# Performance work log

Hardware: AMD Instinct MI355X
Metric: run time of the kernel (lower is better)

## Reference

```python
import jax, jax.numpy as jnp
import numpy as np

CH = 50        # channel
RED = 2        # reduction -> match channels = 25
KS = 3         # ksize
SM_SCALE = 10.0
SCALES = [1.0, 0.9, 0.8, 0.7, 0.6]
ESCAPE_NAN = 1e-4


def prelu(x, a):
    return jnp.where(x >= 0, x, a * x)


def conv1x1(x, w, b):
    # x: [B,Ci,H,W], w: [Co,Ci], b: [Co]
    return jnp.einsum('bihw,oi->bohw', x, w) + b[None, :, None, None]


def patches3(x):
    # extract 3x3 stride-1 SAME patches, torch-unfold (C,kh,kw) ordering
    # x: [B,C,H,W] -> [B, H*W, C, 3, 3]
    B, C, H, W = x.shape
    p = jnp.pad(x, ((0, 0), (0, 0), (1, 1), (1, 1)))
    cols = jnp.stack([p[:, :, i:i + H, j:j + W]
                      for i in range(KS) for j in range(KS)], axis=2)  # [B,C,9,H,W]
    cols = cols.reshape(B, C, KS, KS, H * W)
    return cols.transpose(0, 4, 1, 2, 3)


def setup_inputs() -> dict:
    key = jax.random.key(0)
    ks = jax.random.split(key, 7)
    B, H, W = 4, 48, 48
    f = CH // RED  # 25
    s1 = 1.0 / np.sqrt(CH)
    return {
        'x': jax.random.normal(ks[0], (B, CH, H, W), jnp.float32),
        # conv_match_L_base: 1x1 conv CH->f + PReLU
        'w_base': jax.random.normal(ks[1], (f, CH), jnp.float32) * s1,
        'b_base': jnp.zeros((f,), jnp.float32),
        'a_base': jnp.float32(0.25),
        # conv_match: 1x1 conv CH->f + PReLU
        'w_match': jax.random.normal(ks[2], (f, CH), jnp.float32) * s1,
        'b_match': jnp.zeros((f,), jnp.float32),
        'a_match': jnp.float32(0.25),
        # conv_assembly: 1x1 conv CH->CH + PReLU
        'w_asm': jax.random.normal(ks[3], (CH, CH), jnp.float32) * s1,
        'b_asm': jnp.zeros((CH,), jnp.float32),
        'a_asm': jnp.float32(0.25),
    }


def reference(x, w_base, b_base, a_base, w_match, b_match, a_match,
              w_asm, b_asm, a_asm):
    B, C, H, W = x.shape
    match_base = prelu(conv1x1(x, w_base, b_base), a_base)  # [B,25,H,W]

    w_list, raw_list = [], []
    for s in SCALES:
        if s == 1.0:
            ref = x
        else:
            Hs, Ws = int(H * s), int(W * s)
            ref = jax.image.resize(x, (B, C, Hs, Ws), method='cubic')
        base = prelu(conv1x1(ref, w_asm, b_asm), a_asm)       # [B,C,Hs,Ws]
        raw_list.append(patches3(base))                       # [B,Hs*Ws,C,3,3]
        refm = prelu(conv1x1(ref, w_match, b_match), a_match)  # [B,25,Hs,Ws]
        w_list.append(patches3(refm))                         # [B,Hs*Ws,25,3,3]

    wi = jnp.concatenate(w_list, axis=1)    # [B, L, 25, 3, 3]
    raw = jnp.concatenate(raw_list, axis=1)  # [B, L, C, 3, 3]

    def attend(xb, wb, rb):
        # xb: [25,H,W]; wb: [L,25,3,3]; rb: [L,C,3,3]
        norm = jnp.maximum(
            jnp.sqrt(jnp.sum(wb * wb, axis=(1, 2, 3), keepdims=True)),
            ESCAPE_NAN)
        wn = wb / norm
        score = jax.lax.conv_general_dilated(
            xb[None], wn, (1, 1), [(1, 1), (1, 1)])[0]        # [L,H,W]
        attn = jax.nn.softmax(score * SM_SCALE, axis=0)
        # conv_transpose2d(stride=1, pad=1) == corr with flipped, transposed kernel
        wt = jnp.flip(rb, axis=(2, 3)).transpose(1, 0, 2, 3)  # [C,L,3,3]
        out = jax.lax.conv_general_dilated(
            attn[None], wt, (1, 1), [(1, 1), (1, 1)])[0]      # [C,H,W]
        return out * 0.25

    y = jax.vmap(attend)(match_base, wi, raw)
    return y + x  # res_scale = 1
```

## Files before the change

### kernel.cpp

```cpp
#include <hip/hip_runtime.h>
#include <hip/hip_bf16.h>
#include <math.h>


#define L_TOT 7470
#define L_PAD 7680
#define NCHUNK 4
#define CHUNK_TILES 30
#define KD    256
#define JD    512
#define HW    2304

typedef unsigned short u16;
typedef __attribute__((ext_vector_type(8))) short bf16x8;
typedef __attribute__((ext_vector_type(4))) float f32x4;

__device__ inline u16 f2b(float f) {
    __hip_bfloat16 h = __float2bfloat16(f);
    return __builtin_bit_cast(u16, h);
}
__device__ inline float b2f(u16 u) {
    __hip_bfloat16 h = __builtin_bit_cast(__hip_bfloat16, u);
    return __bfloat162float(h);
}

__constant__ int c_hs[5]   = {48, 43, 38, 33, 28};
__constant__ int c_loff[6] = {0, 2304, 4153, 5597, 6686, 7470};

#define GLOAD16(g, l) __builtin_amdgcn_global_load_lds(                          \
        (__attribute__((address_space(1))) const void*)(g),                      \
        (__attribute__((address_space(3))) void*)(l), 16, 0, 0)

__global__ void prep_kernel(float* __restrict__ wmall, int* __restrict__ dtab) {
    int r = blockIdx.x * 256 + threadIdx.x;
    if (r < 142) {
        int sizes[4] = {43, 38, 33, 28};
        int si = 0, i = r, woffs = 0;
        for (si = 0; si < 4; ++si) {
            if (i < sizes[si]) break;
            i -= sizes[si];
            woffs += sizes[si] * 48;
        }
        int osz = sizes[si];
        float inv_scale = 48.0f / (float)osz;
        float kscale = inv_scale;
        float sample_f = ((float)i + 0.5f) * inv_scale - 0.5f;
        float w[48];
        float tot = 0.f;
        for (int j = 0; j < 48; ++j) {
            float t = fabsf(sample_f - (float)j) / kscale;
            float v;
            if (t >= 2.f)       v = 0.f;
            else if (t >= 1.f)  v = ((-0.5f * t + 2.5f) * t - 4.f) * t + 2.f;
            else                v = ((1.5f * t - 2.5f) * t) * t + 1.f;
            w[j] = v;
            tot += v;
        }
        float invt = 1.f / tot;
        for (int j = 0; j < 48; ++j) wmall[woffs + i * 48 + j] = w[j] * invt;
    }
    if (r < L_PAD) {
        int v;
        if (r >= L_TOT) v = (int)0x80000000u;
        else {
            int si = 0;
#pragma unroll
            for (int s = 0; s < 4; ++s)
                if (r >= c_loff[s + 1]) si = s + 1;
            int pos = r - c_loff[si];
            int hs = c_hs[si];
            int ly = pos / hs, lx = pos % hs;
            v = si | (ly << 4) | (lx << 10);
        }
        dtab[r] = v;
    }
}

__global__ void resize_h_all(const float* __restrict__ in, const float* __restrict__ wm,
                             float* __restrict__ t1, float* __restrict__ t2,
                             float* __restrict__ t3, float* __restrict__ t4) {
    int idx = blockIdx.x * 256 + threadIdx.x;
    int rem = idx, osz, woffm;
    float* tmp;
    if (rem < 200 * 43 * 48) { osz = 43; tmp = t1; woffm = 0; }
    else {
        rem -= 200 * 43 * 48;
        if (rem < 200 * 38 * 48) { osz = 38; tmp = t2; woffm = 43 * 48; }
        else {
            rem -= 200 * 38 * 48;
            if (rem < 200 * 33 * 48) { osz = 33; tmp = t3; woffm = (43 + 38) * 48; }
            else {
                rem -= 200 * 33 * 48;
                if (rem >= 200 * 28 * 48) return;
                osz = 28; tmp = t4; woffm = (43 + 38 + 33) * 48;
            }
        }
    }
    int xi = rem % 48;
    int t = rem / 48;
    int yo = t % osz;
    int bc = t / osz;
    const float* wr = wm + (size_t)(woffm + yo * 48);
    const float* ip = in + (size_t)bc * 2304 + xi;
    float s = 0.f;
#pragma unroll
    for (int yi = 0; yi < 48; ++yi) s += wr[yi] * ip[yi * 48];
    tmp[rem] = s;
}

__global__ void resize_w_all(const float* __restrict__ t1, const float* __restrict__ t2,
                             const float* __restrict__ t3, const float* __restrict__ t4,
                             const float* __restrict__ wm,
                             float* __restrict__ r1, float* __restrict__ r2,
                             float* __restrict__ r3, float* __restrict__ r4) {
    int idx = blockIdx.x * 256 + threadIdx.x;
    int rem = idx, osz, woffm;
    const float* tmp;
    float* outp;
    if (rem < 200 * 43 * 43) { osz = 43; tmp = t1; outp = r1; woffm = 0; }
    else {
        rem -= 200 * 43 * 43;
        if (rem < 200 * 38 * 38) { osz = 38; tmp = t2; outp = r2; woffm = 43 * 48; }
        else {
            rem -= 200 * 38 * 38;
            if (rem < 200 * 33 * 33) { osz = 33; tmp = t3; outp = r3; woffm = (43 + 38) * 48; }
            else {
                rem -= 200 * 33 * 33;
                if (rem >= 200 * 28 * 28) return;
                osz = 28; tmp = t4; outp = r4; woffm = (43 + 38 + 33) * 48;
            }
        }
    }
    int xo = rem % osz;
    int t = rem / osz;
    int yo = t % osz;
    int bc = t / osz;
    const float* wr = wm + (size_t)(woffm + xo * 48);
    const float* ip = tmp + ((size_t)bc * osz + yo) * 48;
    float s = 0.f;
#pragma unroll
    for (int xi = 0; xi < 48; ++xi) s += wr[xi] * ip[xi];
    outp[rem] = s;
}

__global__ void conv_all(const float* __restrict__ x,
                         const float* __restrict__ r1, const float* __restrict__ r2,
                         const float* __restrict__ r3, const float* __restrict__ r4,
                         const float* __restrict__ w_asm, const float* __restrict__ b_asm,
                         const float* __restrict__ a_asm,
                         const float* __restrict__ w_match, const float* __restrict__ b_match,
                         const float* __restrict__ a_match,
                         const float* __restrict__ w_base, const float* __restrict__ b_base,
                         const float* __restrict__ a_base,
                         float* __restrict__ base_out, float* __restrict__ refm_out,
                         float* __restrict__ mb_out) {
    int idx = blockIdx.x * 256 + threadIdx.x;
    int rem = idx, P, loffv, NCO;
    const float* in;
    if (rem < 400 * 2304) { P = 2304; in = x; loffv = 0; NCO = 100; }
    else {
        rem -= 400 * 2304;
        if (rem < 300 * 1849) { P = 1849; in = r1; loffv = 2304; NCO = 75; }
        else {
            rem -= 300 * 1849;
            if (rem < 300 * 1444) { P = 1444; in = r2; loffv = 4153; NCO = 75; }
            else {
                rem -= 300 * 1444;
                if (rem < 300 * 1089) { P = 1089; in = r3; loffv = 5597; NCO = 75; }
                else {
                    rem -= 300 * 1089;
                    if (rem >= 300 * 784) return;
                    P = 784; in = r4; loffv = 6686; NCO = 75;
                }
            }
        }
    }
    int p = rem % P;
    int t = rem / P;
    int co = t % NCO;
    int b = t / NCO;
    const float* ip = in + (size_t)b * 50 * P + p;
    const float* wr;
    float bias, av;
    float* outp;
    if (co < 50) {
        wr = w_asm + co * 50; bias = b_asm[co]; av = a_asm[0];
        outp = base_out + (size_t)200 * loffv + ((size_t)(b * 50 + co)) * P + p;
    } else if (co < 75) {
        int cm = co - 50;
        wr = w_match + cm * 50; bias = b_match[cm]; av = a_match[0];
        outp = refm_out + (size_t)100 * loffv + ((size_t)(b * 25 + cm)) * P + p;
    } else {
        int cm = co - 75;
        wr = w_base + cm * 50; bias = b_base[cm]; av = a_base[0];
        outp = mb_out + ((size_t)(b * 25 + cm)) * P + p;
    }
    float s = bias;
#pragma unroll
    for (int ci = 0; ci < 50; ++ci) s += wr[ci] * ip[(size_t)ci * P];
    *outp = (s >= 0.f) ? s : av * s;
}

__global__ void q_build(const float* __restrict__ mb, u16* __restrict__ Q) {
    int idx = blockIdx.x * 256 + threadIdx.x;
    if (idx >= 4 * HW * 25) return;
    int c = idx % 25;
    int t = idx / 25;
    int p = t % HW;
    int b = t / HW;
    int y = p / 48, xx = p % 48;
    const float* rc = mb + (size_t)(b * 25 + c) * HW;
    u16 ov[9];
#pragma unroll
    for (int ky = 0; ky < 3; ++ky)
#pragma unroll
        for (int kx = 0; kx < 3; ++kx) {
            int yy = y + ky - 1, xv = xx + kx - 1;
            float v = (yy >= 0 && yy < 48 && xv >= 0 && xv < 48) ? rc[yy * 48 + xv] : 0.f;
            ov[ky * 3 + kx] = f2b(v);
        }
    u16* dst = Q + (size_t)(b * HW + p) * KD + c * 9;
#pragma unroll
    for (int r = 0; r < 9; ++r) dst[r] = ov[r];
    if (c == 24) {
        u16* z = dst + 9;
#pragma unroll
        for (int i = 0; i < 31; ++i) z[i] = 0;
    }
}

__global__ void norms_kernel(const float* __restrict__ refm_all, const int* __restrict__ dtab,
                             float* __restrict__ norms) {
    int idx = blockIdx.x * 256 + threadIdx.x;
    if (idx >= 4 * L_PAD) return;
    int l = idx % L_PAD;
    int b = idx / L_PAD;
    int d = dtab[l];
    if (d < 0) return;
    int si = d & 15, ly = (d >> 4) & 63, lx = (d >> 10) & 63;
    int hs = c_hs[si], P = hs * hs;
    const float* rb = refm_all + (size_t)100 * c_loff[si] + (size_t)(b * 25) * P;
    float ss = 0.f;
    for (int c = 0; c < 25; ++c) {
        const float* rc = rb + (size_t)c * P;
#pragma unroll
        for (int ky = 0; ky < 3; ++ky)
#pragma unroll
            for (int kx = 0; kx < 3; ++kx) {
                int yy = ly + ky - 1, xv = lx + kx - 1;
                if (yy >= 0 && yy < hs && xv >= 0 && xv < hs) {
                    float v = rc[yy * hs + xv];
                    ss += v * v;
                }
            }
    }
    norms[(size_t)b * L_PAD + l] = 10.0f / fmaxf(sqrtf(ss), 1e-4f);
}

__global__ void kt_build(const float* __restrict__ refm_all, const int* __restrict__ dtab,
                         const float* __restrict__ norms, u16* __restrict__ K) {
    int idx = blockIdx.x * 256 + threadIdx.x;
    if (idx >= 4 * L_PAD * 25) return;
    int c = idx % 25;
    int t = idx / 25;
    int l = t % L_PAD;
    int b = t / L_PAD;
    u16 ov[9] = {0, 0, 0, 0, 0, 0, 0, 0, 0};
    int d = dtab[l];
    if (d >= 0) {
        int si = d & 15, ly = (d >> 4) & 63, lx = (d >> 10) & 63;
        int hs = c_hs[si], P = hs * hs;
        float nrm = norms[(size_t)b * L_PAD + l];
        const float* rc = refm_all + (size_t)100 * c_loff[si] + (size_t)(b * 25 + c) * P;
#pragma unroll
        for (int ky = 0; ky < 3; ++ky)
#pragma unroll
            for (int kx = 0; kx < 3; ++kx) {
                int yy = ly + ky - 1, xv = lx + kx - 1;
                if (yy >= 0 && yy < hs && xv >= 0 && xv < hs)
                    ov[ky * 3 + kx] = f2b(rc[yy * hs + xv] * nrm);
            }
    }
    u16* dst = K + (size_t)(b * L_PAD + l) * KD + c * 9;
#pragma unroll
    for (int r = 0; r < 9; ++r) dst[r] = ov[r];
    if (c == 24) {
        u16* z = dst + 9;
#pragma unroll
        for (int i = 0; i < 31; ++i) z[i] = 0;
    }
}

__global__ void v_build(const float* __restrict__ base_all, const int* __restrict__ dtab,
                        u16* __restrict__ VT) {
    int idx = blockIdx.x * 256 + threadIdx.x;
    if (idx >= 4 * JD * (L_PAD / 8)) return;
    int l8 = idx % (L_PAD / 8);
    int t = idx / (L_PAD / 8);
    int j = t % JD;
    int b = t / JD;
    int l0 = l8 * 8;
    bf16x8 ov = (bf16x8){0, 0, 0, 0, 0, 0, 0, 0};
    if (j < 450) {
        int c = j / 9, r = j % 9, ky = r / 3, kx = r % 3;
#pragma unroll
        for (int u = 0; u < 8; ++u) {
            int d = dtab[l0 + u];
            float v = 0.f;
            if (d >= 0) {
                int si = d & 15, ly = (d >> 4) & 63, lx = (d >> 10) & 63;
                int hs = c_hs[si], P = hs * hs;
                int yy = ly + ky - 1, xv = lx + kx - 1;
                if (yy >= 0 && yy < hs && xv >= 0 && xv < hs)
                    v = base_all[(size_t)200 * c_loff[si] + (size_t)(b * 50 + c) * P + yy * hs + xv];
            }
            ov[u] = (short)f2b(v);
        }
    }
    *(bf16x8*)&VT[(size_t)(b * JD + j) * L_PAD + l0] = ov;
}

__global__ __launch_bounds__(256, 4) void attn_score(
    const u16* __restrict__ Qg, const u16* __restrict__ Kg,
    u16* __restrict__ Ag, float* __restrict__ mC, float* __restrict__ dC) {
    __shared__ u16 smem[64 * KD];
    __shared__ float sm_m[2][64], sm_d[2][64];
    const int bx = blockIdx.x, by = blockIdx.y;
    const int mt = by % 36, zq = by / 36;
    const int z16 = bx + 8 * zq;
    const int b = z16 >> 2, chunk = z16 & 3;
    const int bm = mt * 64;
    const u16* Q = Qg + (size_t)b * HW * KD;
    const u16* K = Kg + (size_t)b * L_PAD * KD;
    u16* A = Ag + (size_t)b * HW * L_PAD;
    const int tid = threadIdx.x, lane = tid & 63, wid = tid >> 6;
    const int wr = wid >> 1, wc = wid & 1;
    const int l15 = lane & 15, l16 = lane >> 4;
    const int l7 = lane & 7;
    const int r_lo = lane >> 5;
    const int u_dst = lane & 31;

    {
        const u16* qrow = Q + (size_t)(bm + wid * 16 + r_lo) * KD;
        u16* qdst = smem + (size_t)(wid * 16) * KD;
#pragma unroll
        for (int q = 0; q < 8; ++q) {
            int sw = (u_dst ^ ((q * 2 + r_lo) & 7)) * 8;
            GLOAD16(qrow + (size_t)(q * 2) * KD + sw, qdst + (q * 2) * KD);
        }
    }
    __syncthreads();
    bf16x8 qf[2][8];
#pragma unroll
    for (int m = 0; m < 2; ++m)
#pragma unroll
        for (int k = 0; k < 8; ++k)
            qf[m][k] = *(const bf16x8*)&smem[(size_t)(wr * 32 + m * 16 + l15) * KD
                                             + (((k * 4 + l16) ^ l7) * 8)];
    __syncthreads();

    float mrun[2][4];
#pragma unroll
    for (int m = 0; m < 2; ++m)
#pragma unroll
        for (int r = 0; r < 4; ++r) mrun[m][r] = -3e38f;

    const int t0 = chunk * CHUNK_TILES;
    const int colb_base = wc * 32 + l15;

    for (int t = t0; t < t0 + CHUNK_TILES; ++t) {
        {
            const u16* krow = K + (size_t)(t * 64 + wid * 16 + r_lo) * KD;
            u16* kdst = smem + (size_t)(wid * 16) * KD;
#pragma unroll
            for (int q = 0; q < 8; ++q) {
                int sw = (u_dst ^ ((q * 2 + r_lo) & 7)) * 8;
                GLOAD16(krow + (size_t)(q * 2) * KD + sw, kdst + (q * 2) * KD);
            }
        }
        __syncthreads();
        f32x4 acc[2][2];
#pragma unroll
        for (int m = 0; m < 2; ++m)
#pragma unroll
            for (int n = 0; n < 2; ++n) acc[m][n] = (f32x4){0.f, 0.f, 0.f, 0.f};
#pragma unroll
        for (int k = 0; k < 8; ++k) {
            bf16x8 bfr[2];
#pragma unroll
            for (int n = 0; n < 2; ++n)
                bfr[n] = *(const bf16x8*)&smem[(size_t)(wc * 32 + n * 16 + l15) * KD
                                               + (((k * 4 + l16) ^ l7) * 8)];
#pragma unroll
            for (int m = 0; m < 2; ++m)
#pragma unroll
                for (int n = 0; n < 2; ++n)
                    acc[m][n] = __builtin_amdgcn_mfma_f32_16x16x32_bf16(qf[m][k], bfr[n], acc[m][n], 0, 0, 0);
        }
        const int col0 = t * 64 + colb_base;
        const bool v0 = col0 < L_TOT, v1 = col0 + 16 < L_TOT;
#pragma unroll
        for (int m = 0; m < 2; ++m)
#pragma unroll
            for (int r = 0; r < 4; ++r) {
                float s0 = v0 ? acc[m][0][r] : -3e38f;
                float s1 = v1 ? acc[m][1][r] : -3e38f;
                mrun[m][r] = fmaxf(mrun[m][r], fmaxf(s0, s1));
            }
        __syncthreads();
    }

#pragma unroll
    for (int m = 0; m < 2; ++m)
#pragma unroll
        for (int r = 0; r < 4; ++r) {
            float mv = mrun[m][r];
#pragma unroll
            for (int st = 1; st <= 8; st <<= 1)
                mv = fmaxf(mv, __shfl_xor(mv, st));
            mrun[m][r] = mv;
        }
    if (l15 == 0) {
#pragma unroll
        for (int m = 0; m < 2; ++m)
#pragma unroll
            for (int r = 0; r < 4; ++r)
                sm_m[wc][wr * 32 + m * 16 + l16 * 4 + r] = mrun[m][r];
    }
    __syncthreads();
#pragma unroll
    for (int m = 0; m < 2; ++m)
#pragma unroll
        for (int r = 0; r < 4; ++r) {
            int row = wr * 32 + m * 16 + l16 * 4 + r;
            mrun[m][r] = fmaxf(sm_m[0][row], sm_m[1][row]);
        }

    float drun[2][4];
#pragma unroll
    for (int m = 0; m < 2; ++m)
#pragma unroll
        for (int r = 0; r < 4; ++r) drun[m][r] = 0.f;

    for (int t = t0; t < t0 + CHUNK_TILES; ++t) {
        {
            const u16* krow = K + (size_t)(t * 64 + wid * 16 + r_lo) * KD;
            u16* kdst = smem + (size_t)(wid * 16) * KD;
#pragma unroll
            for (int q = 0; q < 8; ++q) {
                int sw = (u_dst ^ ((q * 2 + r_lo) & 7)) * 8;
                GLOAD16(krow + (size_t)(q * 2) * KD + sw, kdst + (q * 2) * KD);
            }
        }
        __syncthreads();
        f32x4 acc[2][2];
#pragma unroll
        for (int m = 0; m < 2; ++m)
#pragma unroll
            for (int n = 0; n < 2; ++n) acc[m][n] = (f32x4){0.f, 0.f, 0.f, 0.f};
#pragma unroll
        for (int k = 0; k < 8; ++k) {
            bf16x8 bfr[2];
#pragma unroll
            for (int n = 0; n < 2; ++n)
                bfr[n] = *(const bf16x8*)&smem[(size_t)(wc * 32 + n * 16 + l15) * KD
                                               + (((k * 4 + l16) ^ l7) * 8)];
#pragma unroll
            for (int m = 0; m < 2; ++m)
#pragma unroll
                for (int n = 0; n < 2; ++n)
                    acc[m][n] = __builtin_amdgcn_mfma_f32_16x16x32_bf16(qf[m][k], bfr[n], acc[m][n], 0, 0, 0);
        }
        const int col0 = t * 64 + colb_base;
#pragma unroll
        for (int m = 0; m < 2; ++m) {
            const int row = bm + wr * 32 + m * 16 + l16 * 4;
#pragma unroll
            for (int n = 0; n < 2; ++n) {
                const int col = col0 + n * 16;
                const bool vld = col < L_TOT;
#pragma unroll
                for (int r = 0; r < 4; ++r) {
                    float w = vld ? __expf(acc[m][n][r] - mrun[m][r]) : 0.f;
                    drun[m][r] += w;
                    A[(size_t)(row + r) * L_PAD + col] = f2b(w);
                }
            }
        }
        __syncthreads();
    }

#pragma unroll
    for (int m = 0; m < 2; ++m)
#pragma unroll
        for (int r = 0; r < 4; ++r) {
            float dv = drun[m][r];
#pragma unroll
            for (int st = 1; st <= 8; st <<= 1)
                dv += __shfl_xor(dv, st);
            drun[m][r] = dv;
        }
    if (l15 == 0) {
#pragma unroll
        for (int m = 0; m < 2; ++m)
#pragma unroll
            for (int r = 0; r < 4; ++r)
                sm_d[wc][wr * 32 + m * 16 + l16 * 4 + r] = drun[m][r];
    }
    __syncthreads();
    if (wc == 0 && l15 == 0) {
#pragma unroll
        for (int m = 0; m < 2; ++m)
#pragma unroll
            for (int r = 0; r < 4; ++r) {
                int row = wr * 32 + m * 16 + l16 * 4 + r;
                size_t o = (size_t)(chunk * 4 + b) * HW + bm + row;
                mC[o] = mrun[m][r];
                dC[o] = sm_d[0][row] + sm_d[1][row];
            }
    }
}

__global__ void combine_stats(const float* __restrict__ mC, const float* __restrict__ dC,
                              float* __restrict__ fac) {
    int idx = blockIdx.x * 256 + threadIdx.x;
    if (idx >= 4 * HW) return;
    int b = idx / HW, p = idx % HW;
    float m[NCHUNK], d[NCHUNK];
#pragma unroll
    for (int c = 0; c < NCHUNK; ++c) {
        size_t o = (size_t)(c * 4 + b) * HW + p;
        m[c] = mC[o]; d[c] = dC[o];
    }
    float mf = m[0];
#pragma unroll
    for (int c = 1; c < NCHUNK; ++c) mf = fmaxf(mf, m[c]);
    float w[NCHUNK], df = 0.f;
#pragma unroll
    for (int c = 0; c < NCHUNK; ++c) { w[c] = __expf(m[c] - mf); df += d[c] * w[c]; }
    float inv = 1.0f / df;
#pragma unroll
    for (int c = 0; c < NCHUNK; ++c) fac[(size_t)(c * 4 + b) * HW + p] = w[c] * inv;
}

__global__ __launch_bounds__(256) void gemm2_kernel(
    const u16* __restrict__ VT0, const u16* __restrict__ A0, u16* __restrict__ C0) {
    __shared__ u16 As[128 * 64];
    __shared__ u16 Bs[128 * 64];
    const int bx = blockIdx.x, by = blockIdx.y;
    const int within = by % 72, zq = by / 72;
    const int mt = within & 3, nt = within >> 2;
    const int z = bx + 8 * zq;
    const int batch = z >> 2, chunk = z & 3;
    const u16* A = VT0 + (size_t)batch * JD * L_PAD + chunk * (CHUNK_TILES * 64);
    const u16* B = A0 + (size_t)batch * HW * L_PAD + chunk * (CHUNK_TILES * 64);
    u16* C = C0 + (size_t)z * JD * HW;
    const int bm = mt * 128, bn = nt * 128;
    const int tid = threadIdx.x, lane = tid & 63, wid = tid >> 6;
    const int wr = wid >> 1, wc = wid & 1;
    const int srow = lane >> 3;
    const int scol = (lane & 7) * 8;

    f32x4 acc[4][4];
#pragma unroll
    for (int i = 0; i < 4; ++i)
#pragma unroll
        for (int j = 0; j < 4; ++j) acc[i][j] = (f32x4){0.f, 0.f, 0.f, 0.f};

    const u16* aG = A + (size_t)(bm + wid * 32 + srow) * L_PAD + scol;
    const u16* bG = B + (size_t)(bn + wid * 32 + srow) * L_PAD + scol;
    u16* aL = As + wid * 32 * 64;
    u16* bL = Bs + wid * 32 * 64;

    for (int t = 0; t < CHUNK_TILES; ++t) {
#pragma unroll
        for (int q = 0; q < 4; ++q) {
            GLOAD16(aG + (size_t)q * 8 * L_PAD, aL + q * 8 * 64);
            GLOAD16(bG + (size_t)q * 8 * L_PAD, bL + q * 8 * 64);
        }
        aG += 64;
        bG += 64;
        __syncthreads();
#pragma unroll
        for (int kc = 0; kc < 64; kc += 32) {
            bf16x8 af[4], bf[4];
#pragma unroll
            for (int m = 0; m < 4; ++m)
                af[m] = *(const bf16x8*)&As[(wr * 64 + m * 16 + (lane & 15)) * 64 + kc + (lane >> 4) * 8];
#pragma unroll
            for (int n = 0; n < 4; ++n)
                bf[n] = *(const bf16x8*)&Bs[(wc * 64 + n * 16 + (lane & 15)) * 64 + kc + (lane >> 4) * 8];
#pragma unroll
            for (int m = 0; m < 4; ++m)
#pragma unroll
                for (int n = 0; n < 4; ++n)
                    acc[m][n] = __builtin_amdgcn_mfma_f32_16x16x32_bf16(af[m], bf[n], acc[m][n], 0, 0, 0);
        }
        __syncthreads();
    }
    const int crow0 = bm + wr * 64 + (lane >> 4) * 4;
    const int ccol = bn + wc * 64 + (lane & 15);
#pragma unroll
    for (int m = 0; m < 4; ++m)
#pragma unroll
        for (int n = 0; n < 4; ++n)
#pragma unroll
            for (int r = 0; r < 4; ++r)
                C[(size_t)(crow0 + m * 16 + r) * HW + ccol + n * 16] = f2b(acc[m][n][r]);
}

__global__ void chunk_reduce(const u16* __restrict__ Zt, const float* __restrict__ fac,
                             u16* __restrict__ Zred) {
    int idx = blockIdx.x * 256 + threadIdx.x;
    int total = 4 * JD * HW / 8;
    if (idx >= total) return;
    int e8 = idx * 8;
    int pp = e8 % HW;
    int row = e8 / HW;
    int b = row / JD;
    float s[8] = {};
#pragma unroll
    for (int ch = 0; ch < NCHUNK; ++ch) {
        const float* fp = fac + (size_t)(ch * 4 + b) * HW + pp;
        bf16x8 zv = *(const bf16x8*)&Zt[((size_t)(b * 4 + ch) * JD + (row % JD)) * HW + pp];
#pragma unroll
        for (int u = 0; u < 8; ++u)
            s[u] += fp[u] * b2f((u16)zv[u]);
    }
    bf16x8 o;
#pragma unroll
    for (int u = 0; u < 8; ++u) o[u] = (short)f2b(s[u]);
    *(bf16x8*)&Zred[(size_t)row * HW + pp] = o;
}

__global__ void final_kernel(const u16* __restrict__ Zred, const float* __restrict__ x,
                             float* __restrict__ out) {
    int idx = blockIdx.x * 256 + threadIdx.x;
    if (idx >= 4 * 50 * HW) return;
    int p = idx % HW;
    int t = idx / HW;
    int c = t % 50;
    int b = t / 50;
    int y = p / 48, xx = p % 48;
    const u16* Zb = Zred + (size_t)b * JD * HW;
    float s = 0.f;
#pragma unroll
    for (int ky = 0; ky < 3; ++ky) {
        int yy = y + ky - 1;
        if (yy < 0 || yy >= 48) continue;
#pragma unroll
        for (int kx = 0; kx < 3; ++kx) {
            int xv = xx + kx - 1;
            if (xv < 0 || xv >= 48) continue;
            int pp = yy * 48 + xv;
            int j = c * 9 + (2 - ky) * 3 + (2 - kx);
            s += b2f(Zb[(size_t)j * HW + pp]);
        }
    }
    size_t o = ((size_t)b * 50 + c) * HW + p;
    out[o] = x[o] + 0.25f * s;
}

extern "C" void kernel_launch(void* const* d_in, const int* in_sizes, int n_in,
                              void* d_out, int out_size, void* d_ws, size_t ws_size,
                              hipStream_t stream) {
    const float* x       = (const float*)d_in[0];
    const float* w_base  = (const float*)d_in[1];
    const float* b_base  = (const float*)d_in[2];
    const float* a_base  = (const float*)d_in[3];
    const float* w_match = (const float*)d_in[4];
    const float* b_match = (const float*)d_in[5];
    const float* a_match = (const float*)d_in[6];
    const float* w_asm   = (const float*)d_in[7];
    const float* b_asm   = (const float*)d_in[8];
    const float* a_asm   = (const float*)d_in[9];
    float* out = (float*)d_out;
    float* ws = (float*)d_ws;
    (void)in_sizes; (void)n_in; (void)out_size; (void)ws_size;

    size_t off = 0;
    auto alloc = [&](size_t n) { size_t o = off; off += (n + 63) & ~(size_t)63; return o; };
    size_t o_wm = alloc(142 * 48);
    size_t o_dtab = alloc(L_PAD);
    size_t o_t1 = alloc((size_t)200 * 43 * 48);
    size_t o_t2 = alloc((size_t)200 * 38 * 48);
    size_t o_t3 = alloc((size_t)200 * 33 * 48);
    size_t o_t4 = alloc((size_t)200 * 28 * 48);
    size_t o_r1 = alloc((size_t)200 * 43 * 43);
    size_t o_r2 = alloc((size_t)200 * 38 * 38);
    size_t o_r3 = alloc((size_t)200 * 33 * 33);
    size_t o_r4 = alloc((size_t)200 * 28 * 28);
    size_t o_base = alloc((size_t)200 * L_TOT);
    size_t o_refm = alloc((size_t)100 * L_TOT);
    size_t o_mb = alloc((size_t)100 * HW);
    size_t o_norms = alloc((size_t)4 * L_PAD);

    size_t o_A = 0;
    size_t o_Q = (size_t)4 * HW * L_PAD / 2;
    size_t o_K = o_Q + (size_t)4 * HW * KD / 2;
    size_t o_VT = o_K + (size_t)4 * L_PAD * KD / 2;
    size_t o_Z = o_VT + (size_t)4 * JD * L_PAD / 2;
    size_t o_mc = o_Z + (size_t)16 * JD * HW / 2;
    size_t o_dc = o_mc + (size_t)16 * HW;
    size_t o_fac = o_dc + (size_t)16 * HW;
    size_t o_zred = o_fac + (size_t)16 * HW;

    u16* Qb = (u16*)(ws + o_Q);
    u16* Kb = (u16*)(ws + o_K);
    u16* VTb = (u16*)(ws + o_VT);
    u16* Ab = (u16*)(ws + o_A);
    u16* Zb = (u16*)(ws + o_Z);
    u16* Zrb = (u16*)(ws + o_zred);
    int* dtab = (int*)(ws + o_dtab);

    prep_kernel<<<(L_PAD + 255) / 256, 256, 0, stream>>>(ws + o_wm, dtab);
    {
        int n = 200 * 48 * (43 + 38 + 33 + 28);
        resize_h_all<<<(n + 255) / 256, 256, 0, stream>>>(x, ws + o_wm, ws + o_t1,
                                                          ws + o_t2, ws + o_t3, ws + o_t4);
    }
    {
        int n = 200 * (43 * 43 + 38 * 38 + 33 * 33 + 28 * 28);
        resize_w_all<<<(n + 255) / 256, 256, 0, stream>>>(ws + o_t1, ws + o_t2, ws + o_t3,
                                                          ws + o_t4, ws + o_wm, ws + o_r1,
                                                          ws + o_r2, ws + o_r3, ws + o_r4);
    }
    {
        int n = 400 * 2304 + 300 * (1849 + 1444 + 1089 + 784);
        conv_all<<<(n + 255) / 256, 256, 0, stream>>>(
            x, ws + o_r1, ws + o_r2, ws + o_r3, ws + o_r4,
            w_asm, b_asm, a_asm, w_match, b_match, a_match, w_base, b_base, a_base,
            ws + o_base, ws + o_refm, ws + o_mb);
    }
    {
        int n = 4 * HW * 25;
        q_build<<<(n + 255) / 256, 256, 0, stream>>>(ws + o_mb, Qb);
    }
    {
        int n = 4 * L_PAD;
        norms_kernel<<<(n + 255) / 256, 256, 0, stream>>>(ws + o_refm, dtab, ws + o_norms);
    }
    {
        int n = 4 * L_PAD * 25;
        kt_build<<<(n + 255) / 256, 256, 0, stream>>>(ws + o_refm, dtab, ws + o_norms, Kb);
    }
    {
        int n = 4 * JD * (L_PAD / 8);
        v_build<<<(n + 255) / 256, 256, 0, stream>>>(ws + o_base, dtab, VTb);
    }

    {
        dim3 g(8, 72, 1);
        attn_score<<<g, 256, 0, stream>>>(Qb, Kb, Ab, ws + o_mc, ws + o_dc);
    }
    combine_stats<<<(4 * HW + 255) / 256, 256, 0, stream>>>(ws + o_mc, ws + o_dc, ws + o_fac);

    {
        dim3 g(8, 144, 1);
        gemm2_kernel<<<g, 256, 0, stream>>>(VTb, Ab, Zb);
    }
    {
        int n = 4 * JD * HW / 8;
        chunk_reduce<<<(n + 255) / 256, 256, 0, stream>>>(Zb, ws + o_fac, Zrb);
    }
    final_kernel<<<(4 * 50 * HW + 255) / 256, 256, 0, stream>>>(Zrb, x, out);
}
```

Measured before the change: 534.1 us.

## Single-pass score kernel storing fp16 raw scores; apply exp inside second GEMM

The score kernel now runs the QK GEMM once, tracking only the per-chunk row max and writing the raw scores as fp16 instead of recomputing them in a second pass for exp and the denominator. The exp(s - max) is applied while staging the score tile into shared memory inside the PV GEMM, with register prefetch of the next tile. The softmax denominator comes from an extra all-ones row (j=450) in VT, so the GEMM produces it. This removes half the score GEMM work at the cost of fp16 score precision, more exp work per gemm2 block, and a register-staged load path in gemm2. The score kernel also uses 32-row tiles instead of 64.

```diff
diff --git a/kernel.cpp b/kernel.cpp
--- a/kernel.cpp
+++ b/kernel.cpp
@@ -1,5 +1,6 @@
 #include <hip/hip_runtime.h>
 #include <hip/hip_bf16.h>
+#include <hip/hip_fp16.h>
 #include <math.h>
 
 
@@ -22,6 +23,14 @@
 __device__ inline float b2f(u16 u) {
     __hip_bfloat16 h = __builtin_bit_cast(__hip_bfloat16, u);
     return __bfloat162float(h);
+}
+__device__ inline u16 f2h(float f) {
+    __half h = __float2half(f);
+    return __builtin_bit_cast(u16, h);
+}
+__device__ inline float h2f(u16 u) {
+    __half h = __builtin_bit_cast(__half, u);
+    return __half2float(h);
 }
 
 __constant__ int c_hs[5]   = {48, 43, 38, 33, 28};
@@ -316,57 +325,52 @@
             }
             ov[u] = (short)f2b(v);
         }
+    } else if (j == 450) {
+        const u16 one = f2b(1.0f);
+#pragma unroll
+        for (int u = 0; u < 8; ++u)
+            ov[u] = (short)(dtab[l0 + u] >= 0 ? one : 0);
     }
     *(bf16x8*)&VT[(size_t)(b * JD + j) * L_PAD + l0] = ov;
 }
 
 __global__ __launch_bounds__(256, 4) void attn_score(
     const u16* __restrict__ Qg, const u16* __restrict__ Kg,
-    u16* __restrict__ Ag, float* __restrict__ mC, float* __restrict__ dC) {
+    u16* __restrict__ SRg, float* __restrict__ mC) {
     __shared__ u16 smem[64 * KD];
-    __shared__ float sm_m[2][64], sm_d[2][64];
+    __shared__ float sm_m[2][32];
     const int bx = blockIdx.x, by = blockIdx.y;
-    const int mt = by % 36, zq = by / 36;
+    const int mt = by % 72, zq = by / 72;
     const int z16 = bx + 8 * zq;
     const int b = z16 >> 2, chunk = z16 & 3;
-    const int bm = mt * 64;
+    const int bm = mt * 32;
     const u16* Q = Qg + (size_t)b * HW * KD;
     const u16* K = Kg + (size_t)b * L_PAD * KD;
-    u16* A = Ag + (size_t)b * HW * L_PAD;
+    u16* SR = SRg + (size_t)b * HW * L_PAD;
     const int tid = threadIdx.x, lane = tid & 63, wid = tid >> 6;
     const int wr = wid >> 1, wc = wid & 1;
-    const int l15 = lane & 15, l16 = lane >> 4;
-    const int l7 = lane & 7;
+    const int l15 = lane & 15, l16 = lane >> 4, l7 = lane & 7;
     const int r_lo = lane >> 5;
     const int u_dst = lane & 31;
 
     {
-        const u16* qrow = Q + (size_t)(bm + wid * 16 + r_lo) * KD;
-        u16* qdst = smem + (size_t)(wid * 16) * KD;
-#pragma unroll
-        for (int q = 0; q < 8; ++q) {
+        const u16* qrow = Q + (size_t)(bm + wid * 8 + r_lo) * KD;
+        u16* qdst = smem + (size_t)(wid * 8) * KD;
+#pragma unroll
+        for (int q = 0; q < 4; ++q) {
             int sw = (u_dst ^ ((q * 2 + r_lo) & 7)) * 8;
             GLOAD16(qrow + (size_t)(q * 2) * KD + sw, qdst + (q * 2) * KD);
         }
     }
     __syncthreads();
-    bf16x8 qf[2][8];
-#pragma unroll
-    for (int m = 0; m < 2; ++m)
-#pragma unroll
-        for (int k = 0; k < 8; ++k)
-            qf[m][k] = *(const bf16x8*)&smem[(size_t)(wr * 32 + m * 16 + l15) * KD
-                                             + (((k * 4 + l16) ^ l7) * 8)];
+    bf16x8 qf[8];
+#pragma unroll
+    for (int k = 0; k < 8; ++k)
+        qf[k] = *(const bf16x8*)&smem[(size_t)(wr * 16 + l15) * KD + (((k * 4 + l16) ^ l7) * 8)];
     __syncthreads();
 
-    float mrun[2][4];
-#pragma unroll
-    for (int m = 0; m < 2; ++m)
-#pragma unroll
-        for (int r = 0; r < 4; ++r) mrun[m][r] = -3e38f;
-
+    float mrun[4] = {-3e38f, -3e38f, -3e38f, -3e38f};
     const int t0 = chunk * CHUNK_TILES;
-    const int colb_base = wc * 32 + l15;
 
     for (int t = t0; t < t0 + CHUNK_TILES; ++t) {
         {
@@ -379,11 +383,9 @@
             }
         }
         __syncthreads();
-        f32x4 acc[2][2];
-#pragma unroll
-        for (int m = 0; m < 2; ++m)
-#pragma unroll
-            for (int n = 0; n < 2; ++n) acc[m][n] = (f32x4){0.f, 0.f, 0.f, 0.f};
+        f32x4 acc[2];
+#pragma unroll
+        for (int n = 0; n < 2; ++n) acc[n] = (f32x4){0.f, 0.f, 0.f, 0.f};
 #pragma unroll
         for (int k = 0; k < 8; ++k) {
             bf16x8 bfr[2];
@@ -392,159 +394,51 @@
                 bfr[n] = *(const bf16x8*)&smem[(size_t)(wc * 32 + n * 16 + l15) * KD
                                                + (((k * 4 + l16) ^ l7) * 8)];
 #pragma unroll
-            for (int m = 0; m < 2; ++m)
-#pragma unroll
-                for (int n = 0; n < 2; ++n)
-                    acc[m][n] = __builtin_amdgcn_mfma_f32_16x16x32_bf16(qf[m][k], bfr[n], acc[m][n], 0, 0, 0);
-        }
-        const int col0 = t * 64 + colb_base;
-        const bool v0 = col0 < L_TOT, v1 = col0 + 16 < L_TOT;
-#pragma unroll
-        for (int m = 0; m < 2; ++m)
+            for (int n = 0; n < 2; ++n)
+                acc[n] = __builtin_amdgcn_mfma_f32_16x16x32_bf16(qf[k], bfr[n], acc[n], 0, 0, 0);
+        }
+        const int col0 = t * 64 + wc * 32 + l15;
+        const int row0 = bm + wr * 16 + l16 * 4;
+#pragma unroll
+        for (int n = 0; n < 2; ++n) {
+            const int col = col0 + n * 16;
+            const bool vld = col < L_TOT;
 #pragma unroll
             for (int r = 0; r < 4; ++r) {
-                float s0 = v0 ? acc[m][0][r] : -3e38f;
-                float s1 = v1 ? acc[m][1][r] : -3e38f;
-                mrun[m][r] = fmaxf(mrun[m][r], fmaxf(s0, s1));
-            }
+                float s = acc[n][r];
+                if (vld) mrun[r] = fmaxf(mrun[r], s);
+                SR[(size_t)(row0 + r) * L_PAD + col] = vld ? f2h(s) : (u16)0xFC00;
+            }
+        }
         __syncthreads();
     }
 
 #pragma unroll
-    for (int m = 0; m < 2; ++m)
-#pragma unroll
-        for (int r = 0; r < 4; ++r) {
-            float mv = mrun[m][r];
-#pragma unroll
-            for (int st = 1; st <= 8; st <<= 1)
-                mv = fmaxf(mv, __shfl_xor(mv, st));
-            mrun[m][r] = mv;
-        }
+    for (int r = 0; r < 4; ++r) {
+        float mv = mrun[r];
+#pragma unroll
+        for (int st = 1; st <= 8; st <<= 1)
+            mv = fmaxf(mv, __shfl_xor(mv, st));
+        mrun[r] = mv;
+    }
     if (l15 == 0) {
 #pragma unroll
-        for (int m = 0; m < 2; ++m)
-#pragma unroll
-            for (int r = 0; r < 4; ++r)
-                sm_m[wc][wr * 32 + m * 16 + l16 * 4 + r] = mrun[m][r];
-    }
-    __syncthreads();
-#pragma unroll
-    for (int m = 0; m < 2; ++m)
-#pragma unroll
-        for (int r = 0; r < 4; ++r) {
-            int row = wr * 32 + m * 16 + l16 * 4 + r;
-            mrun[m][r] = fmaxf(sm_m[0][row], sm_m[1][row]);
-        }
-
-    float drun[2][4];
-#pragma unroll
-    for (int m = 0; m < 2; ++m)
-#pragma unroll
-        for (int r = 0; r < 4; ++r) drun[m][r] = 0.f;
-
-    for (int t = t0; t < t0 + CHUNK_TILES; ++t) {
-        {
-            const u16* krow = K + (size_t)(t * 64 + wid * 16 + r_lo) * KD;
-            u16* kdst = smem + (size_t)(wid * 16) * KD;
-#pragma unroll
-            for (int q = 0; q < 8; ++q) {
-                int sw = (u_dst ^ ((q * 2 + r_lo) & 7)) * 8;
-                GLOAD16(krow + (size_t)(q * 2) * KD + sw, kdst + (q * 2) * KD);
-            }
-        }
-        __syncthreads();
-        f32x4 acc[2][2];
-#pragma unroll
-        for (int m = 0; m < 2; ++m)
-#pragma unroll
-            for (int n = 0; n < 2; ++n) acc[m][n] = (f32x4){0.f, 0.f, 0.f, 0.f};
-#pragma unroll
-        for (int k = 0; k < 8; ++k) {
-            bf16x8 bfr[2];
-#pragma unroll
-            for (int n = 0; n < 2; ++n)
-                bfr[n] = *(const bf16x8*)&smem[(size_t)(wc * 32 + n * 16 + l15) * KD
-                                               + (((k * 4 + l16) ^ l7) * 8)];
-#pragma unroll
-            for (int m = 0; m < 2; ++m)
-#pragma unroll
-                for (int n = 0; n < 2; ++n)
-                    acc[m][n] = __builtin_amdgcn_mfma_f32_16x16x32_bf16(qf[m][k], bfr[n], acc[m][n], 0, 0, 0);
-        }
-        const int col0 = t * 64 + colb_base;
-#pragma unroll
-        for (int m = 0; m < 2; ++m) {
-            const int row = bm + wr * 32 + m * 16 + l16 * 4;
-#pragma unroll
-            for (int n = 0; n < 2; ++n) {
-                const int col = col0 + n * 16;
-                const bool vld = col < L_TOT;
-#pragma unroll
-                for (int r = 0; r < 4; ++r) {
-                    float w = vld ? __expf(acc[m][n][r] - mrun[m][r]) : 0.f;
-                    drun[m][r] += w;
-                    A[(size_t)(row + r) * L_PAD + col] = f2b(w);
-                }
-            }
-        }
-        __syncthreads();
-    }
-
-#pragma unroll
-    for (int m = 0; m < 2; ++m)
-#pragma unroll
-        for (int r = 0; r < 4; ++r) {
-            float dv = drun[m][r];
-#pragma unroll
-            for (int st = 1; st <= 8; st <<= 1)
-                dv += __shfl_xor(dv, st);
-            drun[m][r] = dv;
-        }
-    if (l15 == 0) {
-#pragma unroll
-        for (int m = 0; m < 2; ++m)
-#pragma unroll
-            for (int r = 0; r < 4; ++r)
-                sm_d[wc][wr * 32 + m * 16 + l16 * 4 + r] = drun[m][r];
+        for (int r = 0; r < 4; ++r)
+            sm_m[wc][wr * 16 + l16 * 4 + r] = mrun[r];
     }
     __syncthreads();
     if (wc == 0 && l15 == 0) {
 #pragma unroll
-        for (int m = 0; m < 2; ++m)
-#pragma unroll
-            for (int r = 0; r < 4; ++r) {
-                int row = wr * 32 + m * 16 + l16 * 4 + r;
-                size_t o = (size_t)(chunk * 4 + b) * HW + bm + row;
-                mC[o] = mrun[m][r];
-                dC[o] = sm_d[0][row] + sm_d[1][row];
-            }
-    }
-}
-
-__global__ void combine_stats(const float* __restrict__ mC, const float* __restrict__ dC,
-                              float* __restrict__ fac) {
-    int idx = blockIdx.x * 256 + threadIdx.x;
-    if (idx >= 4 * HW) return;
-    int b = idx / HW, p = idx % HW;
-    float m[NCHUNK], d[NCHUNK];
-#pragma unroll
-    for (int c = 0; c < NCHUNK; ++c) {
-        size_t o = (size_t)(c * 4 + b) * HW + p;
-        m[c] = mC[o]; d[c] = dC[o];
-    }
-    float mf = m[0];
-#pragma unroll
-    for (int c = 1; c < NCHUNK; ++c) mf = fmaxf(mf, m[c]);
-    float w[NCHUNK], df = 0.f;
-#pragma unroll
-    for (int c = 0; c < NCHUNK; ++c) { w[c] = __expf(m[c] - mf); df += d[c] * w[c]; }
-    float inv = 1.0f / df;
-#pragma unroll
-    for (int c = 0; c < NCHUNK; ++c) fac[(size_t)(c * 4 + b) * HW + p] = w[c] * inv;
+        for (int r = 0; r < 4; ++r) {
+            int row = wr * 16 + l16 * 4 + r;
+            mC[(size_t)(chunk * 4 + b) * HW + bm + row] = fmaxf(sm_m[0][row], sm_m[1][row]);
+        }
+    }
 }
 
 __global__ __launch_bounds__(256) void gemm2_kernel(
-    const u16* __restrict__ VT0, const u16* __restrict__ A0, u16* __restrict__ C0) {
+    const u16* __restrict__ VT0, const u16* __restrict__ SR0,
+    const float* __restrict__ mC, u16* __restrict__ C0) {
     __shared__ u16 As[128 * 64];
     __shared__ u16 Bs[128 * 64];
     const int bx = blockIdx.x, by = blockIdx.y;
@@ -553,7 +447,7 @@
     const int z = bx + 8 * zq;
     const int batch = z >> 2, chunk = z & 3;
     const u16* A = VT0 + (size_t)batch * JD * L_PAD + chunk * (CHUNK_TILES * 64);
-    const u16* B = A0 + (size_t)batch * HW * L_PAD + chunk * (CHUNK_TILES * 64);
+    const u16* B = SR0 + (size_t)batch * HW * L_PAD + chunk * (CHUNK_TILES * 64);
     u16* C = C0 + (size_t)z * JD * HW;
     const int bm = mt * 128, bn = nt * 128;
     const int tid = threadIdx.x, lane = tid & 63, wid = tid >> 6;
@@ -561,6 +455,14 @@
     const int srow = lane >> 3;
     const int scol = (lane & 7) * 8;
 
+    float mrow[4];
+    {
+        const float* mp = mC + (size_t)(chunk * 4 + batch) * HW;
+#pragma unroll
+        for (int q = 0; q < 4; ++q)
+            mrow[q] = mp[bn + wid * 32 + srow + q * 8];
+    }
+
     f32x4 acc[4][4];
 #pragma unroll
     for (int i = 0; i < 4; ++i)
@@ -570,16 +472,37 @@
     const u16* aG = A + (size_t)(bm + wid * 32 + srow) * L_PAD + scol;
     const u16* bG = B + (size_t)(bn + wid * 32 + srow) * L_PAD + scol;
     u16* aL = As + wid * 32 * 64;
-    u16* bL = Bs + wid * 32 * 64;
+
+    union U8 { uint4 v; u16 h[8]; };
+    uint4 bv[4];
+#pragma unroll
+    for (int q = 0; q < 4; ++q)
+        bv[q] = *(const uint4*)(bG + (size_t)q * 8 * L_PAD);
+    bG += 64;
 
     for (int t = 0; t < CHUNK_TILES; ++t) {
 #pragma unroll
+        for (int q = 0; q < 4; ++q)
+            GLOAD16(aG + (size_t)q * 8 * L_PAD, aL + q * 8 * 64);
+        aG += 64;
+        uint4 bnext[4];
+        if (t < CHUNK_TILES - 1) {
+#pragma unroll
+            for (int q = 0; q < 4; ++q)
+                bnext[q] = *(const uint4*)(bG + (size_t)q * 8 * L_PAD);
+            bG += 64;
+        }
+#pragma unroll
         for (int q = 0; q < 4; ++q) {
-            GLOAD16(aG + (size_t)q * 8 * L_PAD, aL + q * 8 * 64);
-            GLOAD16(bG + (size_t)q * 8 * L_PAD, bL + q * 8 * 64);
-        }
-        aG += 64;
-        bG += 64;
+            U8 uu; uu.v = bv[q];
+            bf16x8 ob;
+#pragma unroll
+            for (int u = 0; u < 8; ++u) {
+                float e = __expf(h2f(uu.h[u]) - mrow[q]);
+                ob[u] = (short)f2b(e);
+            }
+            *(bf16x8*)&Bs[(size_t)(wid * 32 + srow + q * 8) * 64 + scol] = ob;
+        }
         __syncthreads();
 #pragma unroll
         for (int kc = 0; kc < 64; kc += 32) {
@@ -597,6 +520,8 @@
                     acc[m][n] = __builtin_amdgcn_mfma_f32_16x16x32_bf16(af[m], bf[n], acc[m][n], 0, 0, 0);
         }
         __syncthreads();
+#pragma unroll
+        for (int q = 0; q < 4; ++q) bv[q] = bnext[q];
     }
     const int crow0 = bm + wr * 64 + (lane >> 4) * 4;
     const int ccol = bn + wc * 64 + (lane & 15);
@@ -607,6 +532,28 @@
 #pragma unroll
             for (int r = 0; r < 4; ++r)
                 C[(size_t)(crow0 + m * 16 + r) * HW + ccol + n * 16] = f2b(acc[m][n][r]);
+}
+
+__global__ void combine_stats(const float* __restrict__ mC, const u16* __restrict__ Zt,
+                              float* __restrict__ fac) {
+    int idx = blockIdx.x * 256 + threadIdx.x;
+    if (idx >= 4 * HW) return;
+    int b = idx / HW, p = idx % HW;
+    float m[NCHUNK], d[NCHUNK];
+#pragma unroll
+    for (int c = 0; c < NCHUNK; ++c) {
+        m[c] = mC[(size_t)(c * 4 + b) * HW + p];
+        d[c] = b2f(Zt[((size_t)(b * 4 + c) * JD + 450) * HW + p]);
+    }
+    float mf = m[0];
+#pragma unroll
+    for (int c = 1; c < NCHUNK; ++c) mf = fmaxf(mf, m[c]);
+    float w[NCHUNK], df = 0.f;
+#pragma unroll
+    for (int c = 0; c < NCHUNK; ++c) { w[c] = __expf(m[c] - mf); df += d[c] * w[c]; }
+    float inv = 1.0f / df;
+#pragma unroll
+    for (int c = 0; c < NCHUNK; ++c) fac[(size_t)(c * 4 + b) * HW + p] = w[c] * inv;
 }
 
 __global__ void chunk_reduce(const u16* __restrict__ Zt, const float* __restrict__ fac,
@@ -695,20 +642,19 @@
     size_t o_mb = alloc((size_t)100 * HW);
     size_t o_norms = alloc((size_t)4 * L_PAD);
 
-    size_t o_A = 0;
+    size_t o_SR = 0;
     size_t o_Q = (size_t)4 * HW * L_PAD / 2;
     size_t o_K = o_Q + (size_t)4 * HW * KD / 2;
     size_t o_VT = o_K + (size_t)4 * L_PAD * KD / 2;
     size_t o_Z = o_VT + (size_t)4 * JD * L_PAD / 2;
     size_t o_mc = o_Z + (size_t)16 * JD * HW / 2;
-    size_t o_dc = o_mc + (size_t)16 * HW;
-    size_t o_fac = o_dc + (size_t)16 * HW;
+    size_t o_fac = o_mc + (size_t)16 * HW;
     size_t o_zred = o_fac + (size_t)16 * HW;
 
     u16* Qb = (u16*)(ws + o_Q);
     u16* Kb = (u16*)(ws + o_K);
     u16* VTb = (u16*)(ws + o_VT);
-    u16* Ab = (u16*)(ws + o_A);
+    u16* SRb = (u16*)(ws + o_SR);
     u16* Zb = (u16*)(ws + o_Z);
     u16* Zrb = (u16*)(ws + o_zred);
     int* dtab = (int*)(ws + o_dtab);
@@ -750,15 +696,14 @@
     }
 
     {
-        dim3 g(8, 72, 1);
-        attn_score<<<g, 256, 0, stream>>>(Qb, Kb, Ab, ws + o_mc, ws + o_dc);
-    }
-    combine_stats<<<(4 * HW + 255) / 256, 256, 0, stream>>>(ws + o_mc, ws + o_dc, ws + o_fac);
-
-    {
         dim3 g(8, 144, 1);
-        gemm2_kernel<<<g, 256, 0, stream>>>(VTb, Ab, Zb);
-    }
+        attn_score<<<g, 256, 0, stream>>>(Qb, Kb, SRb, ws + o_mc);
+    }
+    {
+        dim3 g(8, 144, 1);
+        gemm2_kernel<<<g, 256, 0, stream>>>(VTb, SRb, ws + o_mc, Zb);
+    }
+    combine_stats<<<(4 * HW + 255) / 256, 256, 0, stream>>>(ws + o_mc, Zb, ws + o_fac);
     {
         int n = 4 * JD * HW / 8;
         chunk_reduce<<<(n + 255) / 256, 256, 0, stream>>>(Zb, ws + o_fac, Zrb);
```

Result: faster. 495.3 us (-7.3%).
